# Performance work log

Hardware: AMD Instinct MI355X
Metric: run time of the kernel (lower is better)

## Reference

```python
import jax, jax.numpy as jnp
import numpy as np

PATCH = 8
MASK_RATIO = 0.75
B, H, W, C = 64, 512, 512, 3
NPH, NPW = H // PATCH, W // PATCH          # 64, 64
NP_TOT = NPH * NPW                          # 4096
NUM_MASK = int(NP_TOT * MASK_RATIO)         # 3072


def setup_inputs() -> dict:
    key = jax.random.key(0)
    k_img, k_perm = jax.random.split(key)
    images = jax.random.normal(k_img, (B, H, W, C), dtype=jnp.float32)
    # random-without-replacement masked patch indices per image (tf.random.shuffle(idx)[:num_mask])
    perm_keys = jax.random.split(k_perm, B)
    perms = jax.vmap(lambda k: jax.random.permutation(k, NP_TOT))(perm_keys)
    mask_indices = perms[:, :NUM_MASK].astype(jnp.int32)  # [B, NUM_MASK]
    return {"images": images, "mask_indices": mask_indices}


def reference(images, mask_indices):
    # Build per-image flat patch mask: ones with zeros scattered at mask_indices.
    b = images.shape[0]
    mask_flat = jnp.ones((b, NP_TOT), dtype=images.dtype)
    mask_flat = mask_flat.at[jnp.arange(b)[:, None], mask_indices].set(0.0)
    # [B, NPH, NPW] -> nearest-neighbor upsample to [B, H, W, 1] by patch repetition
    mask = mask_flat.reshape(b, NPH, NPW)
    mask = jnp.repeat(jnp.repeat(mask, PATCH, axis=1), PATCH, axis=2)[..., None]
    return images * mask
```

## Files before the change

kernel.cpp:

```cpp
#include <hip/hip_runtime.h>

#define BATCH    64
#define HEIGHT   512
#define WIDTH    512
#define CHAN     3
#define PATCH    8
#define NPH      64
#define NPW      64
#define NP_TOT   4096
#define NUM_MASK 3072

#define PER_IMG4 (HEIGHT * WIDTH * CHAN / 4)
#define PER_ROW4 (WIDTH * CHAN / 4)
#define TOTAL4   (BATCH * PER_IMG4)

__global__ void rm_init_mask(unsigned int* __restrict__ mask32) {
    int i = blockIdx.x * blockDim.x + threadIdx.x;
    if (i < BATCH * NP_TOT / 4) mask32[i] = 0x01010101u;
}

__global__ void rm_scatter_zeros(const int* __restrict__ mask_indices,
                                 unsigned char* __restrict__ mask) {
    int i = blockIdx.x * blockDim.x + threadIdx.x;
    if (i < BATCH * NUM_MASK) {
        int b = i / NUM_MASK;
        int idx = mask_indices[i];
        mask[b * NP_TOT + idx] = (unsigned char)0;
    }
}

__global__ void rm_apply_mask(const float4* __restrict__ in,
                              float4* __restrict__ out,
                              const unsigned char* __restrict__ mask) {
    int tid = blockIdx.x * blockDim.x + threadIdx.x;
    int b  = tid / PER_IMG4;
    int r  = tid - b * PER_IMG4;
    int y  = r / PER_ROW4;
    int x4 = r - y * PER_ROW4;
    int px = x4 / 6;
    int py = y >> 3;
    unsigned char m = mask[b * NP_TOT + (py << 6) + px];
    float4 v = make_float4(0.f, 0.f, 0.f, 0.f);
    if (m) v = in[tid];
    out[tid] = v;
}

extern "C" void kernel_launch(void* const* d_in, const int* in_sizes, int n_in,
                              void* d_out, int out_size, void* d_ws, size_t ws_size,
                              hipStream_t stream) {
    const float* images       = (const float*)d_in[0];
    const int*   mask_indices = (const int*)d_in[1];
    float*       out          = (float*)d_out;
    unsigned char* mask       = (unsigned char*)d_ws;

    rm_init_mask<<<(BATCH * NP_TOT / 4 + 255) / 256, 256, 0, stream>>>(
        (unsigned int*)d_ws);

    rm_scatter_zeros<<<(BATCH * NUM_MASK + 255) / 256, 256, 0, stream>>>(
        mask_indices, mask);

    rm_apply_mask<<<TOTAL4 / 256, 256, 0, stream>>>(
        (const float4*)images, (float4*)out, mask);
}
```

Measured before the change: 317.8 us.

## Fuse mask build into apply kernel using per-block shared-memory mask

Replaces the three kernels (mask init, zero scatter, apply) with a single kernel. Each block rebuilds the full per-image patch mask in shared memory from the indices and then processes a contiguous chunk of its image with a grid-stride-like loop. This removes two launches and the global-memory round trip for the mask. In exchange, every one of the 48 blocks per image redundantly reads 12 KB of indices and scatters them into shared memory.

```diff
diff --git a/kernel.cpp b/kernel.cpp
--- a/kernel.cpp
+++ b/kernel.cpp
@@ -12,37 +12,45 @@
 
 #define PER_IMG4 (HEIGHT * WIDTH * CHAN / 4)
 #define PER_ROW4 (WIDTH * CHAN / 4)
-#define TOTAL4   (BATCH * PER_IMG4)
 
-__global__ void rm_init_mask(unsigned int* __restrict__ mask32) {
-    int i = blockIdx.x * blockDim.x + threadIdx.x;
-    if (i < BATCH * NP_TOT / 4) mask32[i] = 0x01010101u;
-}
+#define BLOCKS_PER_IMG 48
+#define CHUNK4 (PER_IMG4 / BLOCKS_PER_IMG)
+#define ITERS  (CHUNK4 / 256)
 
-__global__ void rm_scatter_zeros(const int* __restrict__ mask_indices,
-                                 unsigned char* __restrict__ mask) {
-    int i = blockIdx.x * blockDim.x + threadIdx.x;
-    if (i < BATCH * NUM_MASK) {
-        int b = i / NUM_MASK;
-        int idx = mask_indices[i];
-        mask[b * NP_TOT + idx] = (unsigned char)0;
+__global__ __launch_bounds__(256)
+void rm_fused(const float4* __restrict__ in,
+              float4* __restrict__ out,
+              const int* __restrict__ mask_indices) {
+    __shared__ unsigned char smask[NP_TOT];
+
+    const int b   = blockIdx.x / BLOCKS_PER_IMG;
+    const int blk = blockIdx.x - b * BLOCKS_PER_IMG;
+    const int t   = threadIdx.x;
+
+    unsigned int* sm32 = (unsigned int*)smask;
+#pragma unroll
+    for (int i = 0; i < 4; ++i) sm32[i * 256 + t] = 0x01010101u;
+    __syncthreads();
+
+    const int* idx = mask_indices + b * NUM_MASK;
+#pragma unroll
+    for (int i = 0; i < 12; ++i) smask[idx[i * 256 + t]] = (unsigned char)0;
+    __syncthreads();
+
+    const int img_base = b * PER_IMG4;
+    int local = blk * CHUNK4 + t;
+#pragma unroll 4
+    for (int i = 0; i < ITERS; ++i) {
+        int l  = local + i * 256;
+        int y  = l / PER_ROW4;
+        int x4 = l - y * PER_ROW4;
+        int px = x4 / 6;
+        int py = y >> 3;
+        unsigned char m = smask[(py << 6) + px];
+        float4 v = make_float4(0.f, 0.f, 0.f, 0.f);
+        if (m) v = in[img_base + l];
+        out[img_base + l] = v;
     }
-}
-
-__global__ void rm_apply_mask(const float4* __restrict__ in,
-                              float4* __restrict__ out,
-                              const unsigned char* __restrict__ mask) {
-    int tid = blockIdx.x * blockDim.x + threadIdx.x;
-    int b  = tid / PER_IMG4;
-    int r  = tid - b * PER_IMG4;
-    int y  = r / PER_ROW4;
-    int x4 = r - y * PER_ROW4;
-    int px = x4 / 6;
-    int py = y >> 3;
-    unsigned char m = mask[b * NP_TOT + (py << 6) + px];
-    float4 v = make_float4(0.f, 0.f, 0.f, 0.f);
-    if (m) v = in[tid];
-    out[tid] = v;
 }
 
 extern "C" void kernel_launch(void* const* d_in, const int* in_sizes, int n_in,
@@ -51,14 +59,7 @@
     const float* images       = (const float*)d_in[0];
     const int*   mask_indices = (const int*)d_in[1];
     float*       out          = (float*)d_out;
-    unsigned char* mask       = (unsigned char*)d_ws;
 
-    rm_init_mask<<<(BATCH * NP_TOT / 4 + 255) / 256, 256, 0, stream>>>(
-        (unsigned int*)d_ws);
-
-    rm_scatter_zeros<<<(BATCH * NUM_MASK + 255) / 256, 256, 0, stream>>>(
-        mask_indices, mask);
-
-    rm_apply_mask<<<TOTAL4 / 256, 256, 0, stream>>>(
-        (const float4*)images, (float4*)out, mask);
+    rm_fused<<<BATCH * BLOCKS_PER_IMG, 256, 0, stream>>>(
+        (const float4*)images, (float4*)out, mask_indices);
 }
```

Result: no change. 320.0 us (+0.7%).
